# Performance work log

Measured on AMD Instinct MI355X. Metric: run time of the kernel, lower is better.

Reference implementation:

```python
import jax, jax.numpy as jnp
import numpy as np

NUM_USERS = 200000
NUM_ITEMS = 100000
EMB_DIM = 64
NUM_EDGES = 3000000


def setup_inputs() -> dict:
    key = jax.random.key(0)
    k1, k2, k3, k4 = jax.random.split(key, 4)
    user_emb = jax.random.normal(k1, (NUM_USERS, EMB_DIM), dtype=jnp.float32)
    item_emb = jax.random.normal(k2, (NUM_ITEMS, EMB_DIM), dtype=jnp.float32)
    src = jax.random.randint(k3, (NUM_EDGES,), 0, NUM_USERS, dtype=jnp.int32)
    dst = jax.random.randint(k4, (NUM_EDGES,), 0, NUM_ITEMS, dtype=jnp.int32)
    return {"user_emb": user_emb, "item_emb": item_emb, "src": src, "dst": dst}


def _mean_agg(x_src, idx_src, idx_dst, n_dst):
    # gather source features along edges, segment-mean into destination nodes
    msg = x_src[idx_src]                                   # [E, D]
    s = jax.ops.segment_sum(msg, idx_dst, num_segments=n_dst)  # [n_dst, D]
    cnt = jax.ops.segment_sum(jnp.ones((idx_dst.shape[0],), x_src.dtype),
                              idx_dst, num_segments=n_dst)      # [n_dst]
    # DGL mean leaves 0 for nodes with no in-edges
    return jnp.where(cnt[:, None] > 0, s / jnp.maximum(cnt, 1)[:, None], 0.0)


def reference(user_emb, item_emb, src, dst):
    n_users = user_emb.shape[0]
    n_items = item_emb.shape[0]

    def layer(u, i):
        # simultaneous bipartite propagation (both use previous-layer inputs)
        i_new = _mean_agg(u, src, dst, n_items)  # items aggregate user neighbors
        u_new = _mean_agg(i, dst, src, n_users)  # users aggregate item neighbors
        return u_new, i_new

    u0, i0 = user_emb, item_emb
    u1, i1 = layer(u0, i0)
    u2, i2 = layer(u1, i1)
    final_user = (u0 + u1 + u2) / 3.0
    final_item = (i0 + i1 + i2) / 3.0
    return final_user, final_item
```

## Files before the change

kernel.cpp:

```cpp
#include <hip/hip_runtime.h>

#define DIM 64
#define NBK 512
#define TEPT 8
#define TSTRIDE 1040
#define LDSBUF 7168

typedef unsigned int uint;
typedef unsigned short ushort;

__device__ __forceinline__ float bf16_lo(uint u) {
    union { uint u; float f; } c; c.u = u << 16; return c.f;
}
__device__ __forceinline__ float bf16_hi(uint u) {
    union { uint u; float f; } c; c.u = u & 0xffff0000u; return c.f;
}
__device__ __forceinline__ uint f2b(float f) {
    union { float f; uint u; } c; c.f = f;
    return (c.u + 0x7fffu + ((c.u >> 16) & 1u)) >> 16;
}

__global__ void cvt_bf16_pitch(const float* __restrict__ in, ushort* __restrict__ out,
                               int n8, int pitch, int off) {
    int k = blockIdx.x * blockDim.x + threadIdx.x;
    if (k >= n8) return;
    int row = k >> 3, g = k & 7;
    const float4* p = (const float4*)in + (size_t)k * 2;
    float4 a = p[0], b = p[1];
    uint4 o;
    o.x = f2b(a.x) | (f2b(a.y) << 16);
    o.y = f2b(a.z) | (f2b(a.w) << 16);
    o.z = f2b(b.x) | (f2b(b.y) << 16);
    o.w = f2b(b.z) | (f2b(b.w) << 16);
    *(uint4*)(out + (size_t)row * pitch + off + g * 8) = o;
}

__global__ __launch_bounds__(256) void bin_chunked(
        const int* __restrict__ src, const int* __restrict__ dst,
        int* __restrict__ table, uint* __restrict__ bins,
        int E, int n_users, int nu_pb, int ni_pb) {
    __shared__ int cnt[2 * NBK];
    __shared__ int lbase[2 * NBK + 1];
    __shared__ int ws[4];
    __shared__ uint ord[4096];
    for (int i = threadIdx.x; i < 2 * NBK; i += 256) cnt[i] = 0;
    __syncthreads();
    int t0 = blockIdx.x * (256 * TEPT) + threadIdx.x;
    uint st[2 * TEPT];
    #pragma unroll
    for (int k = 0; k < TEPT; ++k) {
        int e = t0 + k * 256;
        if (e < E) {
            int s = src[e], t = dst[e];
            int bu = s / nu_pb;
            int bi = t / ni_pb;
            int ou = atomicAdd(&cnt[bu], 1);
            int oi = atomicAdd(&cnt[NBK + bi], 1);
            st[2 * k]     = ((uint)bu << 12) | (uint)ou;
            st[2 * k + 1] = ((uint)(NBK + bi) << 12) | (uint)oi;
        }
    }
    __syncthreads();
    {
        int c0 = threadIdx.x * 4;
        int a0 = cnt[c0], a1 = cnt[c0 + 1], a2 = cnt[c0 + 2], a3 = cnt[c0 + 3];
        int s4 = a0 + a1 + a2 + a3;
        int lane = threadIdx.x & 63, wid = threadIdx.x >> 6;
        int incl = s4;
        #pragma unroll
        for (int off = 1; off < 64; off <<= 1) {
            int t = __shfl_up(incl, off, 64);
            if (lane >= off) incl += t;
        }
        if (lane == 63) ws[wid] = incl;
        __syncthreads();
        int woff = 0;
        for (int w = 0; w < wid; ++w) woff += ws[w];
        int run = woff + incl - s4;
        lbase[c0] = run; run += a0;
        lbase[c0 + 1] = run; run += a1;
        lbase[c0 + 2] = run; run += a2;
        lbase[c0 + 3] = run; run += a3;
        if (threadIdx.x == 255) lbase[2 * NBK] = run;
    }
    __syncthreads();
    int* trow = table + (size_t)blockIdx.x * TSTRIDE;
    for (int i = threadIdx.x; i <= 2 * NBK; i += 256) trow[i] = lbase[i];
    #pragma unroll
    for (int k = 0; k < TEPT; ++k) {
        int e = t0 + k * 256;
        if (e < E) {
            int s = src[e], t = dst[e];
            uint su = st[2 * k], si = st[2 * k + 1];
            int bu = (int)(su >> 12);
            int bi = (int)(si >> 12) - NBK;
            uint wu = (uint)(s - bu * nu_pb) | ((uint)t << 9);
            uint wi = (uint)(t - bi * ni_pb) | ((uint)s << 8);
            ord[lbase[bu] + (int)(su & 4095u)] = wu;
            ord[lbase[NBK + bi] + (int)(si & 4095u)] = wi;
        }
    }
    __syncthreads();
    int tot = lbase[2 * NBK];
    uint* slab = bins + (size_t)blockIdx.x * 4096;
    for (int j = threadIdx.x; j < tot; j += 256)
        slab[j] = ord[j];
}

__global__ __launch_bounds__(256) void bucket_sums(
        const int* __restrict__ table, int* __restrict__ btot, int ntiles) {
    int b = blockIdx.x;
    int s = 0;
    for (int t = threadIdx.x; t < ntiles; t += 256) {
        const int* row = table + (size_t)t * TSTRIDE + b;
        s += row[1] - row[0];
    }
    #pragma unroll
    for (int m = 1; m < 64; m <<= 1) s += __shfl_xor(s, m, 64);
    __shared__ int ws[4];
    int lane = threadIdx.x & 63, wid = threadIdx.x >> 6;
    if (lane == 0) ws[wid] = s;
    __syncthreads();
    if (threadIdx.x == 0) btot[b] = ws[0] + ws[1] + ws[2] + ws[3];
}

__global__ void scan1024(const int* __restrict__ btot, int* __restrict__ bstart,
                         int* __restrict__ deg, int n_nodes, int total) {
    __shared__ int ws[16];
    int lane = threadIdx.x & 63, wid = threadIdx.x >> 6;
    int v = btot[threadIdx.x];
    int incl = v;
    #pragma unroll
    for (int off = 1; off < 64; off <<= 1) {
        int t = __shfl_up(incl, off, 64);
        if (lane >= off) incl += t;
    }
    if (lane == 63) ws[wid] = incl;
    __syncthreads();
    int woff = 0;
    for (int w = 0; w < wid; ++w) woff += ws[w];
    bstart[threadIdx.x] = woff + incl - v;
    if ((int)threadIdx.x == 1023) {
        bstart[1024] = total;
        deg[n_nodes] = total;
    }
}

__global__ __launch_bounds__(256) void fill_node(
        const uint* __restrict__ bins, const int* __restrict__ table,
        const int* __restrict__ bstart, int* __restrict__ deg,
        int* __restrict__ col,
        int n_users, int n_items, int ntiles, int nu_pb, int ni_pb) {
    __shared__ int cur[400];
    __shared__ int ws[4];
    __shared__ int lbuf[LDSBUF];
    int b = blockIdx.x;
    bool user = b < NBK;
    int bb = user ? b : b - NBK;
    int npb = user ? nu_pb : ni_pb;
    int ncnt = user ? n_users : n_items;
    int node0 = bb * npb;
    int nn = min(npb, ncnt - node0);
    if (nn <= 0) return;
    int idx0 = (user ? 0 : n_users) + node0;
    int colbase = bstart[b];
    int nedge = bstart[b + 1] - colbase;
    uint mask = user ? 511u : 255u;
    int shift = user ? 9 : 8;

    for (int i = threadIdx.x; i < nn; i += 256) cur[i] = 0;
    __syncthreads();
    for (int t = threadIdx.x; t < ntiles; t += 256) {
        const int* row = table + (size_t)t * TSTRIDE + b;
        int a = row[0], e2 = row[1];
        const uint* slab = bins + (size_t)t * 4096;
        for (int j = a; j < e2; ++j)
            atomicAdd(&cur[(int)(slab[j] & mask)], 1);
    }
    __syncthreads();
    int CH = (nn + 255) >> 8;
    int c0 = threadIdx.x * CH;
    int s = 0;
    for (int i = 0; i < CH; ++i) {
        int idx = c0 + i;
        if (idx < nn) s += cur[idx];
    }
    int lane = threadIdx.x & 63, wid = threadIdx.x >> 6;
    int incl = s;
    #pragma unroll
    for (int off = 1; off < 64; off <<= 1) {
        int t = __shfl_up(incl, off, 64);
        if (lane >= off) incl += t;
    }
    if (lane == 63) ws[wid] = incl;
    __syncthreads();
    int woff = 0;
    for (int w = 0; w < wid; ++w) woff += ws[w];
    int running = woff + incl - s;
    for (int i = 0; i < CH; ++i) {
        int idx = c0 + i;
        if (idx < nn) {
            int c = cur[idx];
            cur[idx] = running;
            deg[idx0 + idx] = colbase + running;
            running += c;
        }
    }
    __syncthreads();
    if (nedge <= LDSBUF) {
        for (int t = threadIdx.x; t < ntiles; t += 256) {
            const int* row = table + (size_t)t * TSTRIDE + b;
            int a = row[0], e2 = row[1];
            const uint* slab = bins + (size_t)t * 4096;
            for (int j = a; j < e2; ++j) {
                uint w = slab[j];
                int p = atomicAdd(&cur[(int)(w & mask)], 1);
                lbuf[p] = (int)(w >> shift);
            }
        }
        __syncthreads();
        for (int j = threadIdx.x; j < nedge; j += 256)
            col[colbase + j] = lbuf[j];
    } else {
        for (int t = threadIdx.x; t < ntiles; t += 256) {
            const int* row = table + (size_t)t * TSTRIDE + b;
            int a = row[0], e2 = row[1];
            const uint* slab = bins + (size_t)t * 4096;
            for (int j = a; j < e2; ++j) {
                uint w = slab[j];
                int p = atomicAdd(&cur[(int)(w & mask)], 1);
                col[colbase + p] = (int)(w >> shift);
            }
        }
    }
}

template <int COMBINE>
__global__ __launch_bounds__(256) void gather128(
        const ushort* __restrict__ feat,
        const int* __restrict__ ends,
        const int* __restrict__ col,
        const float* __restrict__ x0,
        const ushort* x1, int x1_pitch, int x1_off,
        float* outf,
        ushort* outb, int ob_pitch, int ob_off,
        int n) {
    int node = blockIdx.x * 4 + (threadIdx.x >> 6);
    if (node >= n) return;
    int lane = threadIdx.x & 63;
    int r = lane >> 3, c = lane & 7;
    int beg = ends[node - 1];
    int end = ends[node];
    const ushort* fbase = feat + c * 8;

    float acc[8];
    #pragma unroll
    for (int j = 0; j < 8; ++j) acc[j] = 0.0f;

    for (int e = beg; e < end; e += 16) {
        int i0 = e + r, i1 = e + 8 + r;
        bool ok0 = i0 < end, ok1 = i1 < end;
        int nb0 = col[ok0 ? i0 : beg];
        int nb1 = col[ok1 ? i1 : beg];
        uint4 v0 = *(const uint4*)(fbase + (size_t)nb0 * DIM);
        uint4 v1 = *(const uint4*)(fbase + (size_t)nb1 * DIM);
        if (ok0) {
            acc[0] += bf16_lo(v0.x); acc[1] += bf16_hi(v0.x);
            acc[2] += bf16_lo(v0.y); acc[3] += bf16_hi(v0.y);
            acc[4] += bf16_lo(v0.z); acc[5] += bf16_hi(v0.z);
            acc[6] += bf16_lo(v0.w); acc[7] += bf16_hi(v0.w);
        }
        if (ok1) {
            acc[0] += bf16_lo(v1.x); acc[1] += bf16_hi(v1.x);
            acc[2] += bf16_lo(v1.y); acc[3] += bf16_hi(v1.y);
            acc[4] += bf16_lo(v1.z); acc[5] += bf16_hi(v1.z);
            acc[6] += bf16_lo(v1.w); acc[7] += bf16_hi(v1.w);
        }
    }
    #pragma unroll
    for (int m = 8; m < 64; m <<= 1) {
        #pragma unroll
        for (int j = 0; j < 8; ++j) acc[j] += __shfl_xor(acc[j], m, 64);
    }
    if (r == 0) {
        int d = end - beg;
        float inv = (d > 0) ? 1.0f / (float)d : 0.0f;
        if (COMBINE) {
            size_t base = (size_t)node * DIM + c * 8;
            float4 xa = *(const float4*)(x0 + base);
            float4 xb = *(const float4*)(x0 + base + 4);
            uint4  xq = *(const uint4*)(x1 + (size_t)node * x1_pitch + x1_off + c * 8);
            float4 oa, ob;
            oa.x = (xa.x + bf16_lo(xq.x) + acc[0] * inv) * (1.0f / 3.0f);
            oa.y = (xa.y + bf16_hi(xq.x) + acc[1] * inv) * (1.0f / 3.0f);
            oa.z = (xa.z + bf16_lo(xq.y) + acc[2] * inv) * (1.0f / 3.0f);
            oa.w = (xa.w + bf16_hi(xq.y) + acc[3] * inv) * (1.0f / 3.0f);
            ob.x = (xb.x + bf16_lo(xq.z) + acc[4] * inv) * (1.0f / 3.0f);
            ob.y = (xb.y + bf16_hi(xq.z) + acc[5] * inv) * (1.0f / 3.0f);
            ob.z = (xb.z + bf16_lo(xq.w) + acc[6] * inv) * (1.0f / 3.0f);
            ob.w = (xb.w + bf16_hi(xq.w) + acc[7] * inv) * (1.0f / 3.0f);
            *(float4*)(outf + base)     = oa;
            *(float4*)(outf + base + 4) = ob;
        } else {
            uint4 o;
            o.x = f2b(acc[0] * inv) | (f2b(acc[1] * inv) << 16);
            o.y = f2b(acc[2] * inv) | (f2b(acc[3] * inv) << 16);
            o.z = f2b(acc[4] * inv) | (f2b(acc[5] * inv) << 16);
            o.w = f2b(acc[6] * inv) | (f2b(acc[7] * inv) << 16);
            *(uint4*)(outb + (size_t)node * ob_pitch + ob_off + c * 8) = o;
        }
    }
}

__global__ __launch_bounds__(256) void gather256_combine(
        const ushort* __restrict__ feat,
        const int* __restrict__ ends,
        const int* __restrict__ col,
        const float* __restrict__ x0,
        float* __restrict__ outf,
        ushort* __restrict__ outb,
        int n) {
    int node = blockIdx.x * 4 + (threadIdx.x >> 6);
    if (node >= n) return;
    int lane = threadIdx.x & 63;
    int c = lane & 15, r = lane >> 4;
    int beg = ends[node - 1];
    int end = ends[node];
    const ushort* fbase = feat + c * 8;

    float acc[8];
    #pragma unroll
    for (int j = 0; j < 8; ++j) acc[j] = 0.0f;

    for (int e = beg; e < end; e += 16) {
        int i0 = e + r, i1 = e + 4 + r, i2 = e + 8 + r, i3 = e + 12 + r;
        bool ok0 = i0 < end, ok1 = i1 < end, ok2 = i2 < end, ok3 = i3 < end;
        int nb0 = col[ok0 ? i0 : beg];
        int nb1 = col[ok1 ? i1 : beg];
        int nb2 = col[ok2 ? i2 : beg];
        int nb3 = col[ok3 ? i3 : beg];
        uint4 v0 = *(const uint4*)(fbase + (size_t)nb0 * 128);
        uint4 v1 = *(const uint4*)(fbase + (size_t)nb1 * 128);
        uint4 v2 = *(const uint4*)(fbase + (size_t)nb2 * 128);
        uint4 v3 = *(const uint4*)(fbase + (size_t)nb3 * 128);
        if (ok0) {
            acc[0] += bf16_lo(v0.x); acc[1] += bf16_hi(v0.x);
            acc[2] += bf16_lo(v0.y); acc[3] += bf16_hi(v0.y);
            acc[4] += bf16_lo(v0.z); acc[5] += bf16_hi(v0.z);
            acc[6] += bf16_lo(v0.w); acc[7] += bf16_hi(v0.w);
        }
        if (ok1) {
            acc[0] += bf16_lo(v1.x); acc[1] += bf16_hi(v1.x);
            acc[2] += bf16_lo(v1.y); acc[3] += bf16_hi(v1.y);
            acc[4] += bf16_lo(v1.z); acc[5] += bf16_hi(v1.z);
            acc[6] += bf16_lo(v1.w); acc[7] += bf16_hi(v1.w);
        }
        if (ok2) {
            acc[0] += bf16_lo(v2.x); acc[1] += bf16_hi(v2.x);
            acc[2] += bf16_lo(v2.y); acc[3] += bf16_hi(v2.y);
            acc[4] += bf16_lo(v2.z); acc[5] += bf16_hi(v2.z);
            acc[6] += bf16_lo(v2.w); acc[7] += bf16_hi(v2.w);
        }
        if (ok3) {
            acc[0] += bf16_lo(v3.x); acc[1] += bf16_hi(v3.x);
            acc[2] += bf16_lo(v3.y); acc[3] += bf16_hi(v3.y);
            acc[4] += bf16_lo(v3.z); acc[5] += bf16_hi(v3.z);
            acc[6] += bf16_lo(v3.w); acc[7] += bf16_hi(v3.w);
        }
    }
    #pragma unroll
    for (int m = 16; m < 64; m <<= 1) {
        #pragma unroll
        for (int j = 0; j < 8; ++j) acc[j] += __shfl_xor(acc[j], m, 64);
    }
    float b8[8];
    #pragma unroll
    for (int j = 0; j < 8; ++j) b8[j] = __shfl_xor(acc[j], 8, 64);

    if (r == 0 && c < 8) {
        int d = end - beg;
        float inv = (d > 0) ? 1.0f / (float)d : 0.0f;
        size_t base = (size_t)node * DIM + c * 8;
        float4 xa = *(const float4*)(x0 + base);
        float4 xb = *(const float4*)(x0 + base + 4);
        float i1v[8];
        #pragma unroll
        for (int j = 0; j < 8; ++j) i1v[j] = acc[j] * inv;
        float4 oa, ob;
        oa.x = (xa.x + i1v[0] + b8[0] * inv) * (1.0f / 3.0f);
        oa.y = (xa.y + i1v[1] + b8[1] * inv) * (1.0f / 3.0f);
        oa.z = (xa.z + i1v[2] + b8[2] * inv) * (1.0f / 3.0f);
        oa.w = (xa.w + i1v[3] + b8[3] * inv) * (1.0f / 3.0f);
        ob.x = (xb.x + i1v[4] + b8[4] * inv) * (1.0f / 3.0f);
        ob.y = (xb.y + i1v[5] + b8[5] * inv) * (1.0f / 3.0f);
        ob.z = (xb.z + i1v[6] + b8[6] * inv) * (1.0f / 3.0f);
        ob.w = (xb.w + i1v[7] + b8[7] * inv) * (1.0f / 3.0f);
        *(float4*)(outf + base)     = oa;
        *(float4*)(outf + base + 4) = ob;
        uint4 q;
        q.x = f2b(i1v[0]) | (f2b(i1v[1]) << 16);
        q.y = f2b(i1v[2]) | (f2b(i1v[3]) << 16);
        q.z = f2b(i1v[4]) | (f2b(i1v[5]) << 16);
        q.w = f2b(i1v[6]) | (f2b(i1v[7]) << 16);
        *(uint4*)(outb + base) = q;
    }
}

extern "C" void kernel_launch(void* const* d_in, const int* in_sizes, int n_in,
                              void* d_out, int out_size, void* d_ws, size_t ws_size,
                              hipStream_t stream) {
    const float* u0  = (const float*)d_in[0];
    const float* i0  = (const float*)d_in[1];
    const int*   src = (const int*)d_in[2];
    const int*   dst = (const int*)d_in[3];

    const int n_users = in_sizes[0] / DIM;
    const int n_items = in_sizes[1] / DIM;
    const int E       = in_sizes[2];
    const int n_nodes = n_users + n_items;
    const int nu_pb   = (n_users + NBK - 1) / NBK;
    const int ni_pb   = (n_items + NBK - 1) / NBK;

    const size_t u_elems = (size_t)n_users * DIM;
    const size_t i_elems = (size_t)n_items * DIM;

    int* deg    = (int*)d_ws;
    int* btot   = deg + n_nodes + 1;
    int* bstart = btot + 1024;
    int* col    = bstart + 1028;
    ushort* ib  = (ushort*)(col + 2 * (size_t)E);

    float* out_u = (float*)d_out;
    float* out_i = out_u + u_elems;
    ushort* u01  = (ushort*)d_out;
    int*   table = (int*)d_out;
    uint*  bins  = (uint*)out_i;

    const int BLK = 256;
    const int ntiles = (E + BLK * TEPT - 1) / (BLK * TEPT);

    bin_chunked<<<ntiles, BLK, 0, stream>>>(src, dst, table, bins,
                                            E, n_users, nu_pb, ni_pb);
    bucket_sums<<<2 * NBK, BLK, 0, stream>>>(table, btot, ntiles);
    scan1024<<<1, 1024, 0, stream>>>(btot, bstart, deg, n_nodes, 2 * E);
    fill_node<<<2 * NBK, BLK, 0, stream>>>(bins, table, bstart, deg, col,
                                           n_users, n_items, ntiles, nu_pb, ni_pb);

    cvt_bf16_pitch<<<(int)((u_elems / 8 + BLK - 1) / BLK), BLK, 0, stream>>>(
        u0, u01, (int)(u_elems / 8), 128, 0);
    cvt_bf16_pitch<<<(int)((i_elems / 8 + BLK - 1) / BLK), BLK, 0, stream>>>(
        i0, ib, (int)(i_elems / 8), 64, 0);

    const int ug = (n_users + 3) / 4;
    const int ig = (n_items + 3) / 4;

    gather128<0><<<ug, BLK, 0, stream>>>(ib, deg + 1, col, nullptr,
                                         nullptr, 0, 0, nullptr,
                                         u01, 128, 64, n_users);

    gather256_combine<<<ig, BLK, 0, stream>>>(u01, deg + n_users + 1, col,
                                              i0, out_i, ib, n_items);

    gather128<1><<<ug, BLK, 0, stream>>>(ib, deg + 1, col, u0,
                                         u01, 128, 64, out_u,
                                         nullptr, 0, 0, n_users);
}
```

Baseline: 577.8 us.

## Split fill_node into histogram and placement kernels; unroll gather loop to 32 edges

```diff
diff --git a/kernel.cpp b/kernel.cpp
--- a/kernel.cpp
+++ b/kernel.cpp
@@ -146,13 +146,68 @@
     }
 }
 
-__global__ __launch_bounds__(256) void fill_node(
+__global__ __launch_bounds__(256) void fill_hist(
         const uint* __restrict__ bins, const int* __restrict__ table,
         const int* __restrict__ bstart, int* __restrict__ deg,
+        int n_users, int n_items, int ntiles, int nu_pb, int ni_pb) {
+    __shared__ int cur[400];
+    __shared__ int ws[4];
+    int b = blockIdx.x;
+    bool user = b < NBK;
+    int bb = user ? b : b - NBK;
+    int npb = user ? nu_pb : ni_pb;
+    int ncnt = user ? n_users : n_items;
+    int node0 = bb * npb;
+    int nn = min(npb, ncnt - node0);
+    if (nn <= 0) return;
+    int idx0 = (user ? 0 : n_users) + node0;
+    int colbase = bstart[b];
+    uint mask = user ? 511u : 255u;
+
+    for (int i = threadIdx.x; i < nn; i += 256) cur[i] = 0;
+    __syncthreads();
+    for (int t = threadIdx.x; t < ntiles; t += 256) {
+        const int* row = table + (size_t)t * TSTRIDE + b;
+        int a = row[0], e2 = row[1];
+        const uint* slab = bins + (size_t)t * 4096;
+        for (int j = a; j < e2; ++j)
+            atomicAdd(&cur[(int)(slab[j] & mask)], 1);
+    }
+    __syncthreads();
+    int CH = (nn + 255) >> 8;
+    int c0 = threadIdx.x * CH;
+    int s = 0;
+    for (int i = 0; i < CH; ++i) {
+        int idx = c0 + i;
+        if (idx < nn) s += cur[idx];
+    }
+    int lane = threadIdx.x & 63, wid = threadIdx.x >> 6;
+    int incl = s;
+    #pragma unroll
+    for (int off = 1; off < 64; off <<= 1) {
+        int t = __shfl_up(incl, off, 64);
+        if (lane >= off) incl += t;
+    }
+    if (lane == 63) ws[wid] = incl;
+    __syncthreads();
+    int woff = 0;
+    for (int w = 0; w < wid; ++w) woff += ws[w];
+    int running = woff + incl - s;
+    for (int i = 0; i < CH; ++i) {
+        int idx = c0 + i;
+        if (idx < nn) {
+            deg[idx0 + idx] = colbase + running;
+            running += cur[idx];
+        }
+    }
+}
+
+__global__ __launch_bounds__(256) void fill_place(
+        const uint* __restrict__ bins, const int* __restrict__ table,
+        const int* __restrict__ bstart, const int* __restrict__ deg,
         int* __restrict__ col,
         int n_users, int n_items, int ntiles, int nu_pb, int ni_pb) {
     __shared__ int cur[400];
-    __shared__ int ws[4];
     __shared__ int lbuf[LDSBUF];
     int b = blockIdx.x;
     bool user = b < NBK;
@@ -168,44 +223,8 @@
     uint mask = user ? 511u : 255u;
     int shift = user ? 9 : 8;
 
-    for (int i = threadIdx.x; i < nn; i += 256) cur[i] = 0;
-    __syncthreads();
-    for (int t = threadIdx.x; t < ntiles; t += 256) {
-        const int* row = table + (size_t)t * TSTRIDE + b;
-        int a = row[0], e2 = row[1];
-        const uint* slab = bins + (size_t)t * 4096;
-        for (int j = a; j < e2; ++j)
-            atomicAdd(&cur[(int)(slab[j] & mask)], 1);
-    }
-    __syncthreads();
-    int CH = (nn + 255) >> 8;
-    int c0 = threadIdx.x * CH;
-    int s = 0;
-    for (int i = 0; i < CH; ++i) {
-        int idx = c0 + i;
-        if (idx < nn) s += cur[idx];
-    }
-    int lane = threadIdx.x & 63, wid = threadIdx.x >> 6;
-    int incl = s;
-    #pragma unroll
-    for (int off = 1; off < 64; off <<= 1) {
-        int t = __shfl_up(incl, off, 64);
-        if (lane >= off) incl += t;
-    }
-    if (lane == 63) ws[wid] = incl;
-    __syncthreads();
-    int woff = 0;
-    for (int w = 0; w < wid; ++w) woff += ws[w];
-    int running = woff + incl - s;
-    for (int i = 0; i < CH; ++i) {
-        int idx = c0 + i;
-        if (idx < nn) {
-            int c = cur[idx];
-            cur[idx] = running;
-            deg[idx0 + idx] = colbase + running;
-            running += c;
-        }
-    }
+    for (int i = threadIdx.x; i < nn; i += 256)
+        cur[i] = deg[idx0 + i] - colbase;
     __syncthreads();
     if (nedge <= LDSBUF) {
         for (int t = threadIdx.x; t < ntiles; t += 256) {
@@ -257,13 +276,17 @@
     #pragma unroll
     for (int j = 0; j < 8; ++j) acc[j] = 0.0f;
 
-    for (int e = beg; e < end; e += 16) {
-        int i0 = e + r, i1 = e + 8 + r;
-        bool ok0 = i0 < end, ok1 = i1 < end;
+    for (int e = beg; e < end; e += 32) {
+        int i0 = e + r, i1 = e + 8 + r, i2 = e + 16 + r, i3 = e + 24 + r;
+        bool ok0 = i0 < end, ok1 = i1 < end, ok2 = i2 < end, ok3 = i3 < end;
         int nb0 = col[ok0 ? i0 : beg];
         int nb1 = col[ok1 ? i1 : beg];
+        int nb2 = col[ok2 ? i2 : beg];
+        int nb3 = col[ok3 ? i3 : beg];
         uint4 v0 = *(const uint4*)(fbase + (size_t)nb0 * DIM);
         uint4 v1 = *(const uint4*)(fbase + (size_t)nb1 * DIM);
+        uint4 v2 = *(const uint4*)(fbase + (size_t)nb2 * DIM);
+        uint4 v3 = *(const uint4*)(fbase + (size_t)nb3 * DIM);
         if (ok0) {
             acc[0] += bf16_lo(v0.x); acc[1] += bf16_hi(v0.x);
             acc[2] += bf16_lo(v0.y); acc[3] += bf16_hi(v0.y);
@@ -275,6 +298,18 @@
             acc[2] += bf16_lo(v1.y); acc[3] += bf16_hi(v1.y);
             acc[4] += bf16_lo(v1.z); acc[5] += bf16_hi(v1.z);
             acc[6] += bf16_lo(v1.w); acc[7] += bf16_hi(v1.w);
+        }
+        if (ok2) {
+            acc[0] += bf16_lo(v2.x); acc[1] += bf16_hi(v2.x);
+            acc[2] += bf16_lo(v2.y); acc[3] += bf16_hi(v2.y);
+            acc[4] += bf16_lo(v2.z); acc[5] += bf16_hi(v2.z);
+            acc[6] += bf16_lo(v2.w); acc[7] += bf16_hi(v2.w);
+        }
+        if (ok3) {
+            acc[0] += bf16_lo(v3.x); acc[1] += bf16_hi(v3.x);
+            acc[2] += bf16_lo(v3.y); acc[3] += bf16_hi(v3.y);
+            acc[4] += bf16_lo(v3.z); acc[5] += bf16_hi(v3.z);
+            acc[6] += bf16_lo(v3.w); acc[7] += bf16_hi(v3.w);
         }
     }
     #pragma unroll
@@ -443,8 +478,10 @@
                                             E, n_users, nu_pb, ni_pb);
     bucket_sums<<<2 * NBK, BLK, 0, stream>>>(table, btot, ntiles);
     scan1024<<<1, 1024, 0, stream>>>(btot, bstart, deg, n_nodes, 2 * E);
-    fill_node<<<2 * NBK, BLK, 0, stream>>>(bins, table, bstart, deg, col,
+    fill_hist<<<2 * NBK, BLK, 0, stream>>>(bins, table, bstart, deg,
                                            n_users, n_items, ntiles, nu_pb, ni_pb);
+    fill_place<<<2 * NBK, BLK, 0, stream>>>(bins, table, bstart, deg, col,
+                                            n_users, n_items, ntiles, nu_pb, ni_pb);
 
     cvt_bf16_pitch<<<(int)((u_elems / 8 + BLK - 1) / BLK), BLK, 0, stream>>>(
         u0, u01, (int)(u_elems / 8), 128, 0);
```

Result: no change. 575.4 us (-0.4%).
